# Kernel optimization log

Hardware: AMD Instinct MI355X
Metric: run time of the kernel (lower is better)

## Reference

```python
import jax, jax.numpy as jnp
import numpy as np

N = 50000      # nodes
E = 800000     # edges (before self-loops)
F_IN = 256     # num_features
H = 8          # heads (conv1)
C = 32         # hidden_size per head (conv1)
OUT = 2        # conv2 out channels (1 head)
NEG_SLOPE = 0.2


def setup_inputs() -> dict:
    key = jax.random.key(0)
    ks = jax.random.split(key, 12)
    x = jax.random.normal(ks[0], (N, F_IN), jnp.float32)
    edge_index = jax.random.randint(ks[1], (2, E), 0, N, dtype=jnp.int64)

    def glorot(k, shape):
        fan = shape[0] if len(shape) == 2 else int(np.prod(shape))
        s = float(np.sqrt(6.0 / (fan + shape[-1])))
        return jax.random.uniform(k, shape, jnp.float32, -s, s)

    W1 = glorot(ks[2], (F_IN, H * C))
    att_src1 = glorot(ks[3], (H, C))
    att_dst1 = glorot(ks[4], (H, C))
    b1 = jnp.zeros((H * C,), jnp.float32)
    W2 = glorot(ks[5], (H * C, 1 * OUT))
    att_src2 = glorot(ks[6], (1, OUT))
    att_dst2 = glorot(ks[7], (1, OUT))
    b2 = jnp.zeros((OUT,), jnp.float32)
    return {"x": x, "edge_index": edge_index, "W1": W1, "att_src1": att_src1,
            "att_dst1": att_dst1, "b1": b1, "W2": W2, "att_src2": att_src2,
            "att_dst2": att_dst2, "b2": b2}


def gat_conv(x, src, dst, W, a_src, a_dst, b, heads, ch, n):
    # x: [n, f] -> projected [n, heads, ch]
    xp = (x @ W).reshape(n, heads, ch)
    alpha_src = jnp.einsum('nhc,hc->nh', xp, a_src)   # [n, H]
    alpha_dst = jnp.einsum('nhc,hc->nh', xp, a_dst)   # [n, H]
    e = jax.nn.leaky_relu(alpha_src[src] + alpha_dst[dst], NEG_SLOPE)  # [E', H]
    # segment softmax over edges grouped by destination node
    m = jax.ops.segment_max(e, dst, num_segments=n)                    # [n, H]
    p = jnp.exp(e - m[dst])
    denom = jax.ops.segment_sum(p, dst, num_segments=n)                # [n, H]
    alpha = p / denom[dst]                                             # [E', H]
    # weighted scatter-aggregate of source messages
    out = jax.ops.segment_sum(xp[src] * alpha[:, :, None], dst, num_segments=n)
    return out.reshape(n, heads * ch) + b


def reference(x, edge_index, W1, att_src1, att_dst1, b1, W2, att_src2, att_dst2, b2):
    n = x.shape[0]
    loops = jnp.arange(n, dtype=edge_index.dtype)  # GATConv add_self_loops=True
    src = jnp.concatenate([edge_index[0], loops])
    dst = jnp.concatenate([edge_index[1], loops])
    h = jax.nn.relu(gat_conv(x, src, dst, W1, att_src1, att_dst1, b1, H, C, n))
    # eval mode: F.dropout and attention dropout are identity
    return gat_conv(h, src, dst, W2, att_src2, att_dst2, b2, 1, OUT, n)
```

## Files before the change

### kernel.cpp

```cpp
#include <hip/hip_runtime.h>
#include <math.h>

#define N_NODES 50000
#define N_EDGES 800000
#define EP (N_EDGES + N_NODES)
#define NEG 0.2f
#define SCAN_BLOCKS 49
#define HB N_NODES

typedef __attribute__((ext_vector_type(8))) short bf16x8;
typedef __attribute__((ext_vector_type(4))) float f32x4;
typedef __attribute__((ext_vector_type(2))) float f32x2;

static __device__ __forceinline__ unsigned short bf16_rn(float f) {
    union { float f; unsigned int u; } v; v.f = f;
    unsigned int u = v.u;
    unsigned int r = (u + 0x7FFFu + ((u >> 16) & 1u)) >> 16;
    return (unsigned short)r;
}
static __device__ __forceinline__ f32x2 bf2_unpack(unsigned int u) {
    union { unsigned int i; float f; } a, b;
    a.i = u << 16; b.i = u & 0xFFFF0000u;
    return (f32x2){a.f, b.f};
}


__global__ void k_hist(const int* __restrict__ ei, int* __restrict__ counts) {
    int e = blockIdx.x * 256 + threadIdx.x;
    if (e >= EP) return;
    int d = (e < N_EDGES) ? ei[N_EDGES + e] : (e - N_EDGES);
    atomicAdd(&counts[d], 1);
}

__global__ void k_scan_block(const int* __restrict__ counts, int* __restrict__ excl,
                             int* __restrict__ bsums) {
    __shared__ int wsum[4];
    int b = blockIdx.x, t = threadIdx.x;
    int lane = t & 63, w = t >> 6;
    int i0 = b * 1024 + t * 4;
    int v0 = (i0 + 0 < N_NODES) ? counts[i0 + 0] : 0;
    int v1 = (i0 + 1 < N_NODES) ? counts[i0 + 1] : 0;
    int v2 = (i0 + 2 < N_NODES) ? counts[i0 + 2] : 0;
    int v3 = (i0 + 3 < N_NODES) ? counts[i0 + 3] : 0;
    int s = v0 + v1 + v2 + v3;
    int incl = s;
    #pragma unroll
    for (int d = 1; d < 64; d <<= 1) {
        int u = __shfl_up(incl, d);
        if (lane >= d) incl += u;
    }
    if (lane == 63) wsum[w] = incl;
    __syncthreads();
    if (t == 0) {
        int run = 0;
        #pragma unroll
        for (int i = 0; i < 4; ++i) { int x = wsum[i]; wsum[i] = run; run += x; }
        bsums[b] = run;
    }
    __syncthreads();
    int base = wsum[w] + incl - s;
    if (i0 + 0 < N_NODES) excl[i0 + 0] = base;
    if (i0 + 1 < N_NODES) excl[i0 + 1] = base + v0;
    if (i0 + 2 < N_NODES) excl[i0 + 2] = base + v0 + v1;
    if (i0 + 3 < N_NODES) excl[i0 + 3] = base + v0 + v1 + v2;
}

__global__ void k_scan_add(int* __restrict__ row_ptr, const int* __restrict__ bsums) {
    __shared__ int soff;
    int b = blockIdx.x, t = threadIdx.x;
    if (t < 64) {
        int v = (t < SCAN_BLOCKS) ? bsums[t] : 0;
        int incl = v;
        #pragma unroll
        for (int d = 1; d < 64; d <<= 1) {
            int u = __shfl_up(incl, d);
            if (t >= d) incl += u;
        }
        if (t == b) soff = incl - v;
    }
    __syncthreads();
    int off = soff;
    int i0 = b * 1024 + t * 4;
    #pragma unroll
    for (int j = 0; j < 4; ++j)
        if (i0 + j < N_NODES) row_ptr[i0 + j] += off;
    if (b == 0 && t == 0) row_ptr[N_NODES] = EP;
}

__global__ void k_scatter(const int* __restrict__ ei, const int* __restrict__ row_ptr,
                          int* __restrict__ fill, int* __restrict__ colb) {
    int e = blockIdx.x * 256 + threadIdx.x;
    if (e >= EP) return;
    int s, d;
    if (e < N_EDGES) { s = ei[e]; d = ei[N_EDGES + e]; }
    else             { s = e - N_EDGES; d = s; }
    int pos = row_ptr[d] + atomicAdd(&fill[d], 1);
    colb[pos] = s;
}

__global__ void k_cvtWfrag(const float* __restrict__ W1, bf16x8* __restrict__ Wfrag) {
    int ft = blockIdx.x * 256 + threadIdx.x;
    int c = ft >> 10, rem = ft & 1023;
    int nt = rem >> 6, l = rem & 63;
    int n = (l & 15) * 16 + nt;
    int k0 = c * 32 + (l >> 4) * 8;
    bf16x8 f;
    #pragma unroll
    for (int j = 0; j < 8; ++j)
        f[j] = (short)bf16_rn(W1[(k0 + j) * 256 + n]);
    Wfrag[ft] = f;
}

#define GM_GRID 782
__global__ __launch_bounds__(256) void
k_gemm1m(const float* __restrict__ x, const bf16x8* __restrict__ Wfrag,
         unsigned short* __restrict__ xph,
         const float* __restrict__ asrc, const float* __restrict__ adst,
         float* __restrict__ as1T, float* __restrict__ ad1T) {
    __shared__ bf16x8 lds[1024];
    int t = threadIdx.x, l = t & 63, w = t >> 6;
    int rowbase = blockIdx.x * 64 + w * 16;
    int m = l & 15, kg = l >> 4;

    f32x4 acc[16];
    #pragma unroll
    for (int nt = 0; nt < 16; ++nt)
        acc[nt] = (f32x4){0.f, 0.f, 0.f, 0.f};

    int r0 = rowbase + m;
    if (r0 > N_NODES - 1) r0 = N_NODES - 1;
    const float4* x4 = (const float4*)x;

    for (int c = 0; c < 8; ++c) {
        __syncthreads();
        const bf16x8* src = Wfrag + c * 1024;
        #pragma unroll
        for (int q = 0; q < 4; ++q)
            lds[q * 256 + t] = src[q * 256 + t];
        __syncthreads();

        int kb = (c * 32 + kg * 8) >> 2;
        float4 xa0 = x4[r0 * 64 + kb], xb0 = x4[r0 * 64 + kb + 1];
        bf16x8 aF0;
        aF0[0] = (short)bf16_rn(xa0.x); aF0[1] = (short)bf16_rn(xa0.y);
        aF0[2] = (short)bf16_rn(xa0.z); aF0[3] = (short)bf16_rn(xa0.w);
        aF0[4] = (short)bf16_rn(xb0.x); aF0[5] = (short)bf16_rn(xb0.y);
        aF0[6] = (short)bf16_rn(xb0.z); aF0[7] = (short)bf16_rn(xb0.w);

        #pragma unroll
        for (int nt = 0; nt < 16; ++nt) {
            bf16x8 bF = lds[nt * 64 + l];
            acc[nt] = __builtin_amdgcn_mfma_f32_16x16x32_bf16(aF0, bF, acc[nt], 0, 0, 0);
        }
    }

    int cbase = l & 15, rq = l >> 4;
    int head = cbase >> 1, hhalf = cbase & 1;
    float asV[16], adV[16];
    #pragma unroll
    for (int q = 0; q < 4; ++q) {
        float4 sa = ((const float4*)asrc)[cbase * 4 + q];
        float4 da = ((const float4*)adst)[cbase * 4 + q];
        asV[q * 4 + 0] = sa.x; asV[q * 4 + 1] = sa.y; asV[q * 4 + 2] = sa.z; asV[q * 4 + 3] = sa.w;
        adV[q * 4 + 0] = da.x; adV[q * 4 + 1] = da.y; adV[q * 4 + 2] = da.z; adV[q * 4 + 3] = da.w;
    }
    #pragma unroll
    for (int reg = 0; reg < 4; ++reg) {
        int gr = rowbase + rq * 4 + reg;
        unsigned int ob[8];
        float ps = 0.f, pd = 0.f;
        #pragma unroll
        for (int q = 0; q < 8; ++q) {
            float v0 = acc[2 * q][reg], v1 = acc[2 * q + 1][reg];
            ob[q] = (unsigned int)bf16_rn(v0) | ((unsigned int)bf16_rn(v1) << 16);
            ps = fmaf(v0, asV[2 * q], ps);     ps = fmaf(v1, asV[2 * q + 1], ps);
            pd = fmaf(v0, adV[2 * q], pd);     pd = fmaf(v1, adV[2 * q + 1], pd);
        }
        ps += __shfl_xor(ps, 1);
        pd += __shfl_xor(pd, 1);
        if (gr < N_NODES) {
            uint4* dst = (uint4*)(xph + (head * HB + gr) * 32 + hhalf * 16);
            dst[0] = make_uint4(ob[0], ob[1], ob[2], ob[3]);
            dst[1] = make_uint4(ob[4], ob[5], ob[6], ob[7]);
            if (hhalf == 0) {
                as1T[head * HB + gr] = ps;
                ad1T[head * HB + gr] = pd;
            }
        }
    }
}

#define AGH_GRID (782 * 8)
__global__ __launch_bounds__(256) void
k_aggh(const uint4* __restrict__ xph4, const float* __restrict__ as1T,
       const float* __restrict__ ad1T, const int* __restrict__ row_ptr,
       const int* __restrict__ colb, const float* __restrict__ b1,
       const float* __restrict__ W2, float2* __restrict__ hpart) {
    int t = threadIdx.x, l = t & 63, w = t >> 6;
    int bid = blockIdx.x;
    int h = bid & 7;
    int g = bid >> 3;
    int node = g * 64 + w * 16 + (l >> 2);
    int sub = l & 3;
    bool alive = node < N_NODES;
    int nc = alive ? node : (N_NODES - 1);
    int start = row_ptr[nc], end = row_ptr[nc + 1];
    if (!alive) end = start;
    float adn = ad1T[h * HB + nc];
    const float* asb = as1T + h * HB;
    const uint4* xb = xph4 + (size_t)h * (HB * 4);

    f32x2 a0 = {0.f, 0.f}, a1 = {0.f, 0.f}, a2 = {0.f, 0.f}, a3 = {0.f, 0.f};
    float den = 0.f;

    int j = start;
    if (j < end) {
        int s = colb[j];
        float av = asb[s];
        uint4 r = xb[s * 4 + sub];
        for (++j; j < end; ++j) {
            int s2 = colb[j];
            float av2 = asb[s2];
            uint4 r2 = xb[s2 * 4 + sub];
            float e = av + adn;
            e = (e > 0.f) ? e : NEG * e;
            float p = __expf(e);
            den += p;
            f32x2 q = {p, p};
            a0 += q * bf2_unpack(r.x);
            a1 += q * bf2_unpack(r.y);
            a2 += q * bf2_unpack(r.z);
            a3 += q * bf2_unpack(r.w);
            av = av2; r = r2;
        }
        float e = av + adn;
        e = (e > 0.f) ? e : NEG * e;
        float p = __expf(e);
        den += p;
        f32x2 q = {p, p};
        a0 += q * bf2_unpack(r.x);
        a1 += q * bf2_unpack(r.y);
        a2 += q * bf2_unpack(r.z);
        a3 += q * bf2_unpack(r.w);
    }

    float inv = 1.f / den;
    const float4* b4 = (const float4*)b1;
    float4 ba = b4[h * 8 + sub * 2 + 0];
    float4 bb = b4[h * 8 + sub * 2 + 1];
    float o0 = fmaxf(fmaf(a0[0], inv, ba.x), 0.f);
    float o1 = fmaxf(fmaf(a0[1], inv, ba.y), 0.f);
    float o2 = fmaxf(fmaf(a1[0], inv, ba.z), 0.f);
    float o3 = fmaxf(fmaf(a1[1], inv, ba.w), 0.f);
    float o4 = fmaxf(fmaf(a2[0], inv, bb.x), 0.f);
    float o5 = fmaxf(fmaf(a2[1], inv, bb.y), 0.f);
    float o6 = fmaxf(fmaf(a3[0], inv, bb.z), 0.f);
    float o7 = fmaxf(fmaf(a3[1], inv, bb.w), 0.f);
    const float4* W4 = (const float4*)W2;
    float4 wA = W4[h * 16 + sub * 4 + 0];
    float4 wB = W4[h * 16 + sub * 4 + 1];
    float4 wC = W4[h * 16 + sub * 4 + 2];
    float4 wD = W4[h * 16 + sub * 4 + 3];
    float d0 = o0 * wA.x + o1 * wA.z + o2 * wB.x + o3 * wB.z
             + o4 * wC.x + o5 * wC.z + o6 * wD.x + o7 * wD.z;
    float d1 = o0 * wA.y + o1 * wA.w + o2 * wB.y + o3 * wB.w
             + o4 * wC.y + o5 * wC.w + o6 * wD.y + o7 * wD.w;
    d0 += __shfl_xor(d0, 1);  d0 += __shfl_xor(d0, 2);
    d1 += __shfl_xor(d1, 1);  d1 += __shfl_xor(d1, 2);
    if (sub == 0 && alive)
        hpart[node * 8 + h] = (float2){d0, d1};
}

__global__ void k_post(const float2* __restrict__ hpart, const float* __restrict__ as2w,
                       const float* __restrict__ ad2w, float* __restrict__ xp2,
                       float* __restrict__ as2, float* __restrict__ ad2) {
    int n = blockIdx.x * 256 + threadIdx.x;
    if (n >= N_NODES) return;
    const float4* hp4 = (const float4*)(hpart + n * 8);
    float d0 = 0.f, d1 = 0.f;
    #pragma unroll
    for (int q = 0; q < 4; ++q) {
        float4 v = hp4[q];
        d0 += v.x + v.z;
        d1 += v.y + v.w;
    }
    xp2[2 * n] = d0;
    xp2[2 * n + 1] = d1;
    as2[n] = d0 * as2w[0] + d1 * as2w[1];
    ad2[n] = d0 * ad2w[0] + d1 * ad2w[1];
}

__global__ void k_agg2(const float* __restrict__ xp2, const float* __restrict__ as2,
                       const float* __restrict__ ad2, const int* __restrict__ row_ptr,
                       const int* __restrict__ colb, const float* __restrict__ b2,
                       float* __restrict__ out) {
    int t = threadIdx.x;
    int g = t >> 4, lane = t & 15;
    int n = blockIdx.x * 16 + g;
    int start = row_ptr[n], end = row_ptr[n + 1];
    float adn = ad2[n];
    float a0 = 0.f, a1 = 0.f, den = 0.f;
    for (int j = start + lane; j < end; j += 16) {
        int s = colb[j];
        float e = as2[s] + adn;
        e = (e > 0.f) ? e : NEG * e;
        float p = __expf(e);
        den += p;
        float2 xv = ((const float2*)xp2)[s];
        a0 = fmaf(p, xv.x, a0);
        a1 = fmaf(p, xv.y, a1);
    }
    #pragma unroll
    for (int m = 1; m < 16; m <<= 1) {
        a0 += __shfl_xor(a0, m);
        a1 += __shfl_xor(a1, m);
        den += __shfl_xor(den, m);
    }
    if (lane == 0) {
        out[2 * n] = a0 / den + b2[0];
        out[2 * n + 1] = a1 / den + b2[1];
    }
}

extern "C" void kernel_launch(void* const* d_in, const int* in_sizes, int n_in,
                              void* d_out, int out_size, void* d_ws, size_t ws_size,
                              hipStream_t stream) {
    const float* x     = (const float*)d_in[0];
    const int*   ei    = (const int*)d_in[1];
    const float* W1    = (const float*)d_in[2];
    const float* asrc1 = (const float*)d_in[3];
    const float* adst1 = (const float*)d_in[4];
    const float* b1    = (const float*)d_in[5];
    const float* W2    = (const float*)d_in[6];
    const float* asrc2 = (const float*)d_in[7];
    const float* adst2 = (const float*)d_in[8];
    const float* b2    = (const float*)d_in[9];
    float* out = (float*)d_out;

    char* ws = (char*)d_ws;
    unsigned short* xph = (unsigned short*)(ws + 0);
    bf16x8* Wfrag  = (bf16x8*)(ws + 25600000);
    float2* hpart  = (float2*)(ws + 25800000);
    float* as1T    = (float*)(ws + 102400000);
    float* ad1T    = (float*)(ws + 104000000);
    float* xp2     = (float*)(ws + 105600000);
    float* as2     = (float*)(ws + 106000000);
    float* ad2     = (float*)(ws + 106200000);
    int*   counts  = (int*)  (ws + 106400000);
    int*   fill    = (int*)  (ws + 106600000);
    int*   row_ptr = (int*)  (ws + 106800000);
    int*   colb    = (int*)  (ws + 107000064);
    int*   bsums   = (int*)  (ws + 110400064);

    hipMemsetAsync(counts, 0, 400000, stream);

    int egrid = (EP + 255) / 256;
    k_hist      <<<egrid,       256, 0, stream>>>(ei, counts);
    k_scan_block<<<SCAN_BLOCKS, 256, 0, stream>>>(counts, row_ptr, bsums);
    k_scan_add  <<<SCAN_BLOCKS, 256, 0, stream>>>(row_ptr, bsums);
    k_scatter   <<<egrid,       256, 0, stream>>>(ei, row_ptr, fill, colb);

    k_cvtWfrag  <<<32,     256, 0, stream>>>(W1, Wfrag);
    k_gemm1m   <<<GM_GRID, 256, 0, stream>>>(x, Wfrag, xph, asrc1, adst1, as1T, ad1T);
    k_aggh     <<<AGH_GRID, 256, 0, stream>>>((const uint4*)xph, as1T, ad1T, row_ptr, colb,
                                              b1, W2, hpart);
    k_post     <<<196,     256, 0, stream>>>(hpart, asrc2, adst2, xp2, as2, ad2);
    k_agg2     <<<3125,    256, 0, stream>>>(xp2, as2, ad2, row_ptr, colb, b2, out);
}
```

Before: 324.6 us.

## Share edge index and softmax work across lanes, pack layer-2 node data

In the layer-1 aggregation, each node is handled by four lanes. Before, all four lanes loaded the same colb and attention entries and computed the same exp. Now each lane loads and exponentiates a different edge, and the four lanes broadcast the source index and weight to each other with shuffles, so each edge's gather and exp happens once. This removes redundant scalar loads and transcendental work, but it adds shuffles, drops the one-ahead prefetch of feature rows, and needs a cross-lane reduction of the denominator. Separately, the layer-2 features and attention scalars are packed into one float4 per node, so each edge in k_agg2 needs one gather instead of two or three.

```diff
diff --git a/kernel.cpp b/kernel.cpp
--- a/kernel.cpp
+++ b/kernel.cpp
@@ -202,6 +202,7 @@
     int g = bid >> 3;
     int node = g * 64 + w * 16 + (l >> 2);
     int sub = l & 3;
+    int qb = l & 60;
     bool alive = node < N_NODES;
     int nc = alive ? node : (N_NODES - 1);
     int start = row_ptr[nc], end = row_ptr[nc + 1];
@@ -214,35 +215,40 @@
     float den = 0.f;
 
     int j = start;
+    int s_pf = 0; float av_pf = 0.f; bool v_pf = false;
     if (j < end) {
-        int s = colb[j];
-        float av = asb[s];
-        uint4 r = xb[s * 4 + sub];
-        for (++j; j < end; ++j) {
-            int s2 = colb[j];
-            float av2 = asb[s2];
-            uint4 r2 = xb[s2 * 4 + sub];
-            float e = av + adn;
-            e = (e > 0.f) ? e : NEG * e;
-            float p = __expf(e);
-            den += p;
-            f32x2 q = {p, p};
+        int jj = j + sub;
+        v_pf = jj < end;
+        s_pf = colb[v_pf ? jj : (end - 1)];
+        av_pf = asb[s_pf];
+    }
+    while (j < end) {
+        int s_cur = s_pf; float av_cur = av_pf; bool v_cur = v_pf;
+        j += 4;
+        if (j < end) {
+            int jj = j + sub;
+            v_pf = jj < end;
+            s_pf = colb[v_pf ? jj : (end - 1)];
+            av_pf = asb[s_pf];
+        }
+        float e = av_cur + adn;
+        e = (e > 0.f) ? e : NEG * e;
+        float p = v_cur ? __expf(e) : 0.f;
+        den += p;
+        #pragma unroll
+        for (int eidx = 0; eidx < 4; ++eidx) {
+            int   se = __shfl(s_cur, qb + eidx);
+            float pe = __shfl(p,     qb + eidx);
+            uint4 r = xb[(size_t)se * 4 + sub];
+            f32x2 q = {pe, pe};
             a0 += q * bf2_unpack(r.x);
             a1 += q * bf2_unpack(r.y);
             a2 += q * bf2_unpack(r.z);
             a3 += q * bf2_unpack(r.w);
-            av = av2; r = r2;
-        }
-        float e = av + adn;
-        e = (e > 0.f) ? e : NEG * e;
-        float p = __expf(e);
-        den += p;
-        f32x2 q = {p, p};
-        a0 += q * bf2_unpack(r.x);
-        a1 += q * bf2_unpack(r.y);
-        a2 += q * bf2_unpack(r.z);
-        a3 += q * bf2_unpack(r.w);
-    }
+        }
+    }
+    den += __shfl_xor(den, 1);
+    den += __shfl_xor(den, 2);
 
     float inv = 1.f / den;
     const float4* b4 = (const float4*)b1;
@@ -272,8 +278,7 @@
 }
 
 __global__ void k_post(const float2* __restrict__ hpart, const float* __restrict__ as2w,
-                       const float* __restrict__ ad2w, float* __restrict__ xp2,
-                       float* __restrict__ as2, float* __restrict__ ad2) {
+                       const float* __restrict__ ad2w, float4* __restrict__ pk) {
     int n = blockIdx.x * 256 + threadIdx.x;
     if (n >= N_NODES) return;
     const float4* hp4 = (const float4*)(hpart + n * 8);
@@ -284,31 +289,32 @@
         d0 += v.x + v.z;
         d1 += v.y + v.w;
     }
-    xp2[2 * n] = d0;
-    xp2[2 * n + 1] = d1;
-    as2[n] = d0 * as2w[0] + d1 * as2w[1];
-    ad2[n] = d0 * ad2w[0] + d1 * ad2w[1];
-}
-
-__global__ void k_agg2(const float* __restrict__ xp2, const float* __restrict__ as2,
-                       const float* __restrict__ ad2, const int* __restrict__ row_ptr,
+    float4 r;
+    r.x = d0;
+    r.y = d1;
+    r.z = d0 * as2w[0] + d1 * as2w[1];
+    r.w = d0 * ad2w[0] + d1 * ad2w[1];
+    pk[n] = r;
+}
+
+__global__ void k_agg2(const float4* __restrict__ pk, const int* __restrict__ row_ptr,
                        const int* __restrict__ colb, const float* __restrict__ b2,
                        float* __restrict__ out) {
     int t = threadIdx.x;
     int g = t >> 4, lane = t & 15;
     int n = blockIdx.x * 16 + g;
     int start = row_ptr[n], end = row_ptr[n + 1];
-    float adn = ad2[n];
+    float adn = pk[n].w;
     float a0 = 0.f, a1 = 0.f, den = 0.f;
     for (int j = start + lane; j < end; j += 16) {
         int s = colb[j];
-        float e = as2[s] + adn;
+        float4 r = pk[s];
+        float e = r.z + adn;
         e = (e > 0.f) ? e : NEG * e;
         float p = __expf(e);
         den += p;
-        float2 xv = ((const float2*)xp2)[s];
-        a0 = fmaf(p, xv.x, a0);
-        a1 = fmaf(p, xv.y, a1);
+        a0 = fmaf(p, r.x, a0);
+        a1 = fmaf(p, r.y, a1);
     }
     #pragma unroll
     for (int m = 1; m < 16; m <<= 1) {
@@ -343,9 +349,7 @@
     float2* hpart  = (float2*)(ws + 25800000);
     float* as1T    = (float*)(ws + 102400000);
     float* ad1T    = (float*)(ws + 104000000);
-    float* xp2     = (float*)(ws + 105600000);
-    float* as2     = (float*)(ws + 106000000);
-    float* ad2     = (float*)(ws + 106200000);
+    float4* pk     = (float4*)(ws + 105600000);
     int*   counts  = (int*)  (ws + 106400000);
     int*   fill    = (int*)  (ws + 106600000);
     int*   row_ptr = (int*)  (ws + 106800000);
@@ -364,6 +368,6 @@
     k_gemm1m   <<<GM_GRID, 256, 0, stream>>>(x, Wfrag, xph, asrc1, adst1, as1T, ad1T);
     k_aggh     <<<AGH_GRID, 256, 0, stream>>>((const uint4*)xph, as1T, ad1T, row_ptr, colb,
                                               b1, W2, hpart);
-    k_post     <<<196,     256, 0, stream>>>(hpart, asrc2, adst2, xp2, as2, ad2);
-    k_agg2     <<<3125,    256, 0, stream>>>(xp2, as2, ad2, row_ptr, colb, b2, out);
-}
+    k_post     <<<196,     256, 0, stream>>>(hpart, asrc2, adst2, pk);
+    k_agg2     <<<3125,    256, 0, stream>>>(pk, row_ptr, colb, b2, out);
+}
```

New measurement: 297.8 us. -8.2%, faster.
